# Kernel tuning notes

Measured on AMD Instinct MI355X. Metric: run time of the kernel, lower is better.

Reference implementation:

```python
import jax, jax.numpy as jnp
import numpy as np

EPS = 1e-5  # torch BatchNorm1d default eps
HEADS = 4


def knn_idx(pcd, K):
    # pcd: (B, N, C). Torch: topk of negative squared distance -> nearest K (includes self).
    aa = jnp.sum(pcd * pcd, axis=-1)                       # (B, N)
    inner = jnp.einsum('bnc,bmc->bnm', pcd, pcd)           # (B, N, N)
    pd = 2.0 * inner - aa[:, :, None] - aa[:, None, :]     # = -||a-b||^2
    return jax.lax.top_k(pd, K)[1]                         # (B, N, K) int32


def batchnorm1d(x, gamma, beta):
    # training-mode BN over (B, C, N): stats over batch and point dims, biased var
    m = jnp.mean(x, axis=(0, 2), keepdims=True)
    v = jnp.var(x, axis=(0, 2), keepdims=True)
    return (x - m) * jax.lax.rsqrt(v + EPS) * gamma[None, :, None] + beta[None, :, None]


def setup_inputs() -> dict:
    key = jax.random.key(0)
    ks = jax.random.split(key, 8)
    B, C, N = 4, 64, 8192
    FF = 4 * C  # 256
    x = jax.random.normal(ks[0], (B, C, N), dtype=jnp.float32)
    s = 1.0 / np.sqrt(C).astype(np.float32)
    Wq = jax.random.normal(ks[1], (C, C), dtype=jnp.float32) * s
    Wk = jax.random.normal(ks[2], (C, C), dtype=jnp.float32) * s
    Wv = jax.random.normal(ks[3], (C, C), dtype=jnp.float32) * s
    W1 = jax.random.normal(ks[4], (FF, C), dtype=jnp.float32) * s
    W2 = jax.random.normal(ks[5], (C, FF), dtype=jnp.float32) * (1.0 / np.sqrt(FF).astype(np.float32))
    g1 = jnp.ones((C,), jnp.float32); b1 = jnp.zeros((C,), jnp.float32)
    g2 = jnp.ones((C,), jnp.float32); b2 = jnp.zeros((C,), jnp.float32)
    return {'x': x, 'Wq': Wq, 'Wk': Wk, 'Wv': Wv, 'W1': W1, 'W2': W2,
            'g1': g1, 'b1': b1, 'g2': g2, 'b2': b2, 'K': 40}


def reference(x, Wq, Wk, Wv, W1, W2, g1, b1, g2, b2, K):
    B, C, N = x.shape
    H = HEADS
    D = C // H
    pcd = jnp.transpose(x, (0, 2, 1))                      # (B, N, C)
    idx = knn_idx(pcd, K)                                  # (B, N, K)
    nbr = jax.vmap(lambda p, i: p[i])(pcd, idx)            # (B, N, K, C) gather
    diff = nbr - pcd[:, :, None, :]                        # group_type='diff'
    # 1x1 conv projections
    q = jnp.einsum('oc,bnc->bno', Wq, pcd)                 # (B, N, C)
    k = jnp.einsum('oc,bnkc->bnko', Wk, diff)              # (B, N, K, C)
    v = jnp.einsum('oc,bnkc->bnko', Wv, diff)
    # split heads: channel = (H D), H-major
    qh = q.reshape(B, N, H, D)
    kh = k.reshape(B, N, K, H, D)
    vh = v.reshape(B, N, K, H, D)
    scale = np.float32(np.sqrt(D))
    energy = jnp.einsum('bnhd,bnkhd->bnhk', qh, kh) / scale
    attn = jax.nn.softmax(energy, axis=-1)
    out = jnp.einsum('bnhk,bnkhd->bnhd', attn, vh)         # (B, N, H, D)
    tmp = jnp.transpose(out.reshape(B, N, C), (0, 2, 1))   # (B, C, N)
    x1 = batchnorm1d(x + tmp, g1, b1)
    h = jax.nn.leaky_relu(jnp.einsum('oc,bcn->bon', W1, x1), 0.2)
    ff = jnp.einsum('co,bon->bcn', W2, h)
    return batchnorm1d(x1 + ff, g2, b2)
```

## Files before the change

kernel.cpp:

```cpp
#include <hip/hip_runtime.h>

#define Bc 4
#define Cc 64
#define Nc 8192
#define Kc 40
#define CN (Cc * Nc)

__global__ __launch_bounds__(256) void aa_kernel(const float* __restrict__ x,
                                                 float* __restrict__ aa) {
  const int e = blockIdx.x * 256 + threadIdx.x;
  const int b = e >> 13, n = e & 8191;
  const float* xb = x + (size_t)b * CN + n;
  float s = 0.f;
#pragma unroll
  for (int c = 0; c < 64; ++c) {
    const float v = xb[c * Nc];
    s = fmaf(v, v, s);
  }
  aa[e] = s;
}

__global__ __launch_bounds__(256) void proj_kernel(
    const float* __restrict__ x, const float* __restrict__ Wq,
    const float* __restrict__ Wk, const float* __restrict__ Wv,
    float* __restrict__ qp, float* __restrict__ kp, float* __restrict__ vp) {
  __shared__ float xs[64 * 64];
  __shared__ float wt[64 * 64];
  const int t = threadIdx.x;
  const int w = t >> 6, lane = t & 63;
  const int b = blockIdx.x >> 7;
  const int n0 = (blockIdx.x & 127) << 6;
  const float* xb = x + (size_t)b * CN;
  for (int c = w; c < 64; c += 4) xs[c * 64 + lane] = xb[c * Nc + n0 + lane];

  const float* Ws[3] = {Wq, Wk, Wv};
  float* Ds[3] = {qp, kp, vp};
  for (int mtx = 0; mtx < 3; ++mtx) {
    __syncthreads();
    const float* W = Ws[mtx];
    for (int q = t; q < 4096; q += 256) {
      const int o = q & 63, c = q >> 6;
      wt[c * 64 + o] = W[o * 64 + c];
    }
    __syncthreads();
    float acc[16];
#pragma unroll
    for (int k = 0; k < 16; ++k) acc[k] = 0.f;
#pragma unroll 8
    for (int c = 0; c < 64; ++c) {
      const float xv = xs[c * 64 + lane];
      const float4 w0 = *(const float4*)&wt[c * 64 + w * 16 + 0];
      const float4 w1 = *(const float4*)&wt[c * 64 + w * 16 + 4];
      const float4 w2 = *(const float4*)&wt[c * 64 + w * 16 + 8];
      const float4 w3 = *(const float4*)&wt[c * 64 + w * 16 + 12];
      acc[0] = fmaf(xv, w0.x, acc[0]);   acc[1] = fmaf(xv, w0.y, acc[1]);
      acc[2] = fmaf(xv, w0.z, acc[2]);   acc[3] = fmaf(xv, w0.w, acc[3]);
      acc[4] = fmaf(xv, w1.x, acc[4]);   acc[5] = fmaf(xv, w1.y, acc[5]);
      acc[6] = fmaf(xv, w1.z, acc[6]);   acc[7] = fmaf(xv, w1.w, acc[7]);
      acc[8] = fmaf(xv, w2.x, acc[8]);   acc[9] = fmaf(xv, w2.y, acc[9]);
      acc[10] = fmaf(xv, w2.z, acc[10]); acc[11] = fmaf(xv, w2.w, acc[11]);
      acc[12] = fmaf(xv, w3.x, acc[12]); acc[13] = fmaf(xv, w3.y, acc[13]);
      acc[14] = fmaf(xv, w3.z, acc[14]); acc[15] = fmaf(xv, w3.w, acc[15]);
    }
    float* dst = Ds[mtx] + ((size_t)(b * Nc + n0 + lane)) * 64 + w * 16;
    *(float4*)(dst + 0) = make_float4(acc[0], acc[1], acc[2], acc[3]);
    *(float4*)(dst + 4) = make_float4(acc[4], acc[5], acc[6], acc[7]);
    *(float4*)(dst + 8) = make_float4(acc[8], acc[9], acc[10], acc[11]);
    *(float4*)(dst + 12) = make_float4(acc[12], acc[13], acc[14], acc[15]);
  }
}

__global__ __launch_bounds__(256, 1) void knn_kernel(const float* __restrict__ x,
                                                     const float* __restrict__ aa,
                                                     int* __restrict__ knn) {
  __shared__ float rowT[64][128];
  __shared__ float colT[64][128];
  __shared__ float qv[128][64];
  __shared__ unsigned short qidx[128][64];
  __shared__ float thrS[128][2];
  __shared__ int qcnt[128];

  const int t = threadIdx.x;
  const int ty = t >> 4;
  const int tx = t & 15;
  const int b = blockIdx.x >> 6;
  const int i0 = (blockIdx.x & 63) << 7;
  const float* xb = x + (size_t)b * CN;
  const float* aab = aa + b * Nc;

  if (t < 128) { qcnt[t] = 0; thrS[t][0] = -INFINITY; thrS[t][1] = -INFINITY; }

  const int cSub = t >> 4;
  const int chunk = t & 15;
  for (int cc = 0; cc < 4; ++cc) {
    const int c = cc * 16 + cSub;
    const float* src = xb + (size_t)c * Nc + i0 + chunk * 8;
    const float4 v0 = ((const float4*)src)[0];
    const float4 v1 = ((const float4*)src)[1];
    *(float4*)&rowT[c][chunk * 8] = v0;
    *(float4*)&rowT[c][chunk * 8 + 4] = v1;
  }

  float rA[8];
  {
    const float4 r0 = *(const float4*)&aab[i0 + ty * 8];
    const float4 r1 = *(const float4*)&aab[i0 + ty * 8 + 4];
    rA[0] = r0.x; rA[1] = r0.y; rA[2] = r0.z; rA[3] = r0.w;
    rA[4] = r1.x; rA[5] = r1.y; rA[6] = r1.z; rA[7] = r1.w;
  }

  float lv[40]; int li[40];
#pragma unroll
  for (int q = 0; q < 40; ++q) { lv[q] = -INFINITY; li[q] = 0; }
  float lmin = -INFINITY; int lminpos = 0;

  const int dr = t >> 1, slot = t & 1;

  auto insert = [&](float v, int idx) {
#pragma unroll
    for (int q = 0; q < 40; ++q)
      if (q == lminpos) { lv[q] = v; li[q] = idx; }
    float nm = lv[0]; int np = 0;
#pragma unroll
    for (int q = 1; q < 40; ++q) {
      if (lv[q] < nm) { nm = lv[q]; np = q; }
    }
    lmin = nm; lminpos = np;
  };

  for (int jt = 0; jt < 64; ++jt) {
    const int j0 = jt << 7;
    for (int cc = 0; cc < 4; ++cc) {
      const int c = cc * 16 + cSub;
      const float* src = xb + (size_t)c * Nc + j0 + chunk * 8;
      const float4 v0 = ((const float4*)src)[0];
      const float4 v1 = ((const float4*)src)[1];
      *(float4*)&colT[c][chunk * 8] = v0;
      *(float4*)&colT[c][chunk * 8 + 4] = v1;
    }
    __syncthreads();

    float acc[8][8];
#pragma unroll
    for (int i = 0; i < 8; ++i)
#pragma unroll
      for (int jj = 0; jj < 8; ++jj) acc[i][jj] = 0.f;

#pragma unroll 2
    for (int c = 0; c < 64; ++c) {
      const float4 a0 = *(const float4*)&rowT[c][ty * 8];
      const float4 a1 = *(const float4*)&rowT[c][ty * 8 + 4];
      const float4 b0 = *(const float4*)&colT[c][tx * 4];
      const float4 b1 = *(const float4*)&colT[c][64 + tx * 4];
      const float av[8] = {a0.x, a0.y, a0.z, a0.w, a1.x, a1.y, a1.z, a1.w};
      const float bv[8] = {b0.x, b0.y, b0.z, b0.w, b1.x, b1.y, b1.z, b1.w};
#pragma unroll
      for (int i = 0; i < 8; ++i)
#pragma unroll
        for (int jj = 0; jj < 8; ++jj)
          acc[i][jj] = fmaf(av[i], bv[jj], acc[i][jj]);
    }

    float cA[8];
    {
      const float4 c0 = *(const float4*)&aab[j0 + tx * 4];
      const float4 c1 = *(const float4*)&aab[j0 + 64 + tx * 4];
      cA[0] = c0.x; cA[1] = c0.y; cA[2] = c0.z; cA[3] = c0.w;
      cA[4] = c1.x; cA[5] = c1.y; cA[6] = c1.z; cA[7] = c1.w;
    }

    for (int half = 0; half < 2; ++half) {
      float th8[8];
      {
        const float4* tp = (const float4*)&thrS[ty * 8][0];
        const float4 u0 = tp[0], u1 = tp[1], u2 = tp[2], u3 = tp[3];
        th8[0] = fminf(u0.x, u0.y); th8[1] = fminf(u0.z, u0.w);
        th8[2] = fminf(u1.x, u1.y); th8[3] = fminf(u1.z, u1.w);
        th8[4] = fminf(u2.x, u2.y); th8[5] = fminf(u2.z, u2.w);
        th8[6] = fminf(u3.x, u3.y); th8[7] = fminf(u3.z, u3.w);
      }
#pragma unroll
      for (int i = 0; i < 8; ++i) {
        const int r = ty * 8 + i;
#pragma unroll
        for (int jq = 0; jq < 4; ++jq) {
          const int jj = half * 4 + jq;
          const float v = 2.0f * acc[i][jj] - rA[i] - cA[jj];
          if (v > th8[i]) {
            const int pos = atomicAdd(&qcnt[r], 1);
            qv[r][pos] = v;
            qidx[r][pos] = (unsigned short)(j0 + half * 64 + tx * 4 + jq);
          }
        }
      }
      __syncthreads();
      {
        int cnt = qcnt[dr]; if (cnt > 64) cnt = 64;
        for (int e = slot; e < cnt; e += 2) {
          const float v = qv[dr][e];
          if (v > lmin) insert(v, (int)qidx[dr][e]);
        }
        if (slot == 0) qcnt[dr] = 0;
        thrS[dr][slot] = lmin;
      }
      __syncthreads();
    }
  }

  if (slot == 1) {
#pragma unroll
    for (int q = 0; q < 40; ++q) {
      qv[dr][q] = lv[q];
      qidx[dr][q] = (unsigned short)li[q];
    }
  }
  __syncthreads();
  if (slot == 0) {
#pragma unroll
    for (int q = 0; q < 40; ++q) {
      const float v = qv[dr][q];
      if (v > lmin) insert(v, (int)qidx[dr][q]);
    }
    int* dst = knn + (size_t)(b * Nc + i0 + dr) * Kc;
#pragma unroll
    for (int q = 0; q < 40; ++q) dst[q] = li[q];
  }
}

__global__ __launch_bounds__(256) void attn_kernel(
    const float* __restrict__ x, const float* __restrict__ qp,
    const float* __restrict__ kp, const float* __restrict__ vp,
    const int* __restrict__ knn, float* __restrict__ y) {
  const int lane = threadIdx.x & 63;
  const int wid = threadIdx.x >> 6;
  const int pt = (blockIdx.x << 2) + wid;
  const int b = pt >> 13;
  const int nn = pt & 8191;
  const float q = qp[(size_t)pt * 64 + lane];
  const float vself = vp[(size_t)pt * 64 + lane];
  const float* kpb = kp + (size_t)b * (Nc * 64);
  const float* vpb = vp + (size_t)b * (Nc * 64);
  const int* idn = knn + (size_t)pt * Kc;
  float e[40], vv[40];
#pragma unroll
  for (int j = 0; j < 40; ++j) {
    const int ij = idn[j];
    const float kj = kpb[ij * 64 + lane];
    vv[j] = vpb[ij * 64 + lane];
    float p = q * kj;
    p += __shfl_xor(p, 1);
    p += __shfl_xor(p, 2);
    p += __shfl_xor(p, 4);
    p += __shfl_xor(p, 8);
    e[j] = p * 0.25f;
  }
  float m = e[0];
#pragma unroll
  for (int j = 1; j < 40; ++j) m = fmaxf(m, e[j]);
  float s = 0.f;
#pragma unroll
  for (int j = 0; j < 40; ++j) { e[j] = __expf(e[j] - m); s += e[j]; }
  const float inv = 1.f / s;
  float acc = 0.f;
#pragma unroll
  for (int j = 0; j < 40; ++j) acc = fmaf(e[j] * inv, vv[j], acc);
  const size_t xi = (size_t)b * CN + (size_t)lane * Nc + nn;
  y[xi] = x[xi] + (acc - vself);
}

__global__ __launch_bounds__(256) void stats_kernel(const float* __restrict__ src,
                                                    float* __restrict__ out) {
  const int c = blockIdx.x;
  float s = 0.f, s2 = 0.f;
  for (int b = 0; b < Bc; ++b) {
    const float* p = src + (size_t)b * CN + (size_t)c * Nc;
    for (int i = threadIdx.x; i < Nc; i += 256) {
      const float v = p[i];
      s += v;
      s2 = fmaf(v, v, s2);
    }
  }
  __shared__ float rs[256], rs2[256];
  rs[threadIdx.x] = s; rs2[threadIdx.x] = s2;
  __syncthreads();
  for (int st = 128; st > 0; st >>= 1) {
    if (threadIdx.x < st) {
      rs[threadIdx.x] += rs[threadIdx.x + st];
      rs2[threadIdx.x] += rs2[threadIdx.x + st];
    }
    __syncthreads();
  }
  if (threadIdx.x == 0) {
    const float mean = rs[0] * (1.f / 32768.f);
    const float var = rs2[0] * (1.f / 32768.f) - mean * mean;
    out[c] = mean;
    out[64 + c] = 1.f / sqrtf(var + 1e-5f);
  }
}

__global__ __launch_bounds__(256) void w2t_kernel(const float* __restrict__ W2,
                                                  float* __restrict__ W2t) {
  const int e = blockIdx.x * 256 + threadIdx.x;
  const int o = e >> 6, c = e & 63;
  W2t[e] = W2[c * 256 + o];
}

__global__ __launch_bounds__(256) void ffn_kernel(
    const float* __restrict__ y, const float* __restrict__ W1,
    const float* __restrict__ W2t, const float* __restrict__ st1,
    const float* __restrict__ g1, const float* __restrict__ b1,
    float* __restrict__ z) {
  const int pt = blockIdx.x * 256 + threadIdx.x;
  const int b = pt >> 13, nn = pt & 8191;
  const float* yb = y + (size_t)b * CN + nn;
  float x1[64], z0[64];
#pragma unroll
  for (int c = 0; c < 64; ++c) {
    const float sc = st1[64 + c] * g1[c];
    x1[c] = (yb[(size_t)c * Nc] - st1[c]) * sc + b1[c];
    z0[c] = x1[c];
  }
  for (int o = 0; o < 256; ++o) {
    const float* w1r = W1 + o * 64;
    float hv = 0.f;
#pragma unroll
    for (int c = 0; c < 64; ++c) hv = fmaf(w1r[c], x1[c], hv);
    hv = hv >= 0.f ? hv : 0.2f * hv;
    const float* w2r = W2t + o * 64;
#pragma unroll
    for (int c = 0; c < 64; ++c) z0[c] = fmaf(w2r[c], hv, z0[c]);
  }
  float* zb = z + (size_t)b * CN + nn;
#pragma unroll
  for (int c = 0; c < 64; ++c) zb[(size_t)c * Nc] = z0[c];
}

__global__ __launch_bounds__(256) void bn_apply_kernel(
    const float* __restrict__ z, const float* __restrict__ st2,
    const float* __restrict__ g2, const float* __restrict__ b2,
    float* __restrict__ out) {
  const int e = blockIdx.x * 256 + threadIdx.x;
  const int c = (e >> 13) & 63;
  const float sc = st2[64 + c] * g2[c];
  out[e] = (z[e] - st2[c]) * sc + b2[c];
}

extern "C" void kernel_launch(void* const* d_in, const int* in_sizes, int n_in,
                              void* d_out, int out_size, void* d_ws, size_t ws_size,
                              hipStream_t stream) {
  (void)in_sizes; (void)n_in; (void)out_size; (void)ws_size;
  const float* x  = (const float*)d_in[0];
  const float* Wq = (const float*)d_in[1];
  const float* Wk = (const float*)d_in[2];
  const float* Wv = (const float*)d_in[3];
  const float* W1 = (const float*)d_in[4];
  const float* W2 = (const float*)d_in[5];
  const float* g1 = (const float*)d_in[6];
  const float* b1 = (const float*)d_in[7];
  const float* g2 = (const float*)d_in[8];
  const float* b2 = (const float*)d_in[9];
  float* out = (float*)d_out;

  float* ws = (float*)d_ws;
  float* aa  = ws;
  float* qp  = aa + 32768;
  float* kp  = qp + 2097152;
  float* vp  = kp + 2097152;
  float* y   = vp + 2097152;
  float* z   = y + 2097152;
  float* st1 = z + 2097152;
  float* st2 = st1 + 128;
  float* W2t = st2 + 128;
  int* knn   = (int*)(W2t + 16384);

  hipLaunchKernelGGL(aa_kernel, dim3(128), dim3(256), 0, stream, x, aa);
  hipLaunchKernelGGL(proj_kernel, dim3(512), dim3(256), 0, stream, x, Wq, Wk, Wv, qp, kp, vp);
  hipLaunchKernelGGL(knn_kernel, dim3(256), dim3(256), 0, stream, x, aa, knn);
  hipLaunchKernelGGL(attn_kernel, dim3(8192), dim3(256), 0, stream, x, qp, kp, vp, knn, y);
  hipLaunchKernelGGL(stats_kernel, dim3(64), dim3(256), 0, stream, y, st1);
  hipLaunchKernelGGL(w2t_kernel, dim3(64), dim3(256), 0, stream, W2, W2t);
  hipLaunchKernelGGL(ffn_kernel, dim3(128), dim3(256), 0, stream, y, W1, W2t, st1, g1, b1, z);
  hipLaunchKernelGGL(stats_kernel, dim3(64), dim3(256), 0, stream, z, st2);
  hipLaunchKernelGGL(bn_apply_kernel, dim3(8192), dim3(256), 0, stream, z, st2, g2, b2, out);
}
```

Measured before the change: 1.840 ms.

## Split KNN search over column halves with merge kernel, prefetch and wave-level queues

Splits the KNN search so each block scans half of the candidate columns, which doubles the grid to 512 blocks and allows two blocks per CU. Partial top-40 lists go to scratch memory reused from the y and z buffers, and a new merge kernel combines them. Inside the loop, the next column tile is prefetched into registers. Candidate insertion now builds a per-thread bitmask, drains it in eight rounds separated by wave barriers instead of block barriers, and uses smaller per-row queues. The cost is extra global traffic and a launch for the merge, plus heavier register pressure under launch_bounds(256,2). The 16-entry queue also relies on each round adding at most 16 candidates per row.

New measurement: 3.208 ms. 1.74x slower.

```diff
diff --git a/kernel.cpp b/kernel.cpp
--- a/kernel.cpp
+++ b/kernel.cpp
@@ -70,35 +70,39 @@
   }
 }
 
-__global__ __launch_bounds__(256, 1) void knn_kernel(const float* __restrict__ x,
+__global__ __launch_bounds__(256, 2) void knn_kernel(const float* __restrict__ x,
                                                      const float* __restrict__ aa,
-                                                     int* __restrict__ knn) {
+                                                     float* __restrict__ part_v,
+                                                     unsigned short* __restrict__ part_i) {
   __shared__ float rowT[64][128];
   __shared__ float colT[64][128];
-  __shared__ float qv[128][64];
-  __shared__ unsigned short qidx[128][64];
+  __shared__ float qv[128][16];
+  __shared__ unsigned short qidx[128][16];
   __shared__ float thrS[128][2];
   __shared__ int qcnt[128];
 
   const int t = threadIdx.x;
   const int ty = t >> 4;
   const int tx = t & 15;
-  const int b = blockIdx.x >> 6;
-  const int i0 = (blockIdx.x & 63) << 7;
+  const int blk = blockIdx.x;
+  const int h = blk & 1;
+  const int i0 = ((blk >> 1) & 63) << 7;
+  const int b = blk >> 7;
+  const int j0base = h * 4096;
   const float* xb = x + (size_t)b * CN;
   const float* aab = aa + b * Nc;
 
   if (t < 128) { qcnt[t] = 0; thrS[t][0] = -INFINITY; thrS[t][1] = -INFINITY; }
 
-  const int cSub = t >> 4;
-  const int chunk = t & 15;
-  for (int cc = 0; cc < 4; ++cc) {
-    const int c = cc * 16 + cSub;
-    const float* src = xb + (size_t)c * Nc + i0 + chunk * 8;
-    const float4 v0 = ((const float4*)src)[0];
-    const float4 v1 = ((const float4*)src)[1];
-    *(float4*)&rowT[c][chunk * 8] = v0;
-    *(float4*)&rowT[c][chunk * 8 + 4] = v1;
+#pragma unroll
+  for (int k = 0; k < 8; ++k) {
+    const int c = k * 8 + (t >> 5), j = (t & 31) * 4;
+    *(float4*)&rowT[c][j] = *(const float4*)&xb[(size_t)c * Nc + i0 + j];
+  }
+#pragma unroll
+  for (int k = 0; k < 8; ++k) {
+    const int c = k * 8 + (t >> 5), j = (t & 31) * 4;
+    *(float4*)&colT[c][j] = *(const float4*)&xb[(size_t)c * Nc + j0base + j];
   }
 
   float rA[8];
@@ -113,7 +117,6 @@
 #pragma unroll
   for (int q = 0; q < 40; ++q) { lv[q] = -INFINITY; li[q] = 0; }
   float lmin = -INFINITY; int lminpos = 0;
-
   const int dr = t >> 1, slot = t & 1;
 
   auto insert = [&](float v, int idx) {
@@ -128,17 +131,20 @@
     lmin = nm; lminpos = np;
   };
 
-  for (int jt = 0; jt < 64; ++jt) {
-    const int j0 = jt << 7;
-    for (int cc = 0; cc < 4; ++cc) {
-      const int c = cc * 16 + cSub;
-      const float* src = xb + (size_t)c * Nc + j0 + chunk * 8;
-      const float4 v0 = ((const float4*)src)[0];
-      const float4 v1 = ((const float4*)src)[1];
-      *(float4*)&colT[c][chunk * 8] = v0;
-      *(float4*)&colT[c][chunk * 8 + 4] = v1;
-    }
-    __syncthreads();
+  __syncthreads();
+
+  for (int jt = 0; jt < 32; ++jt) {
+    const int j0 = j0base + (jt << 7);
+
+    float4 pf[8];
+    if (jt < 31) {
+      const int nj0 = j0 + 128;
+#pragma unroll
+      for (int k = 0; k < 8; ++k) {
+        const int c = k * 8 + (t >> 5), j = (t & 31) * 4;
+        pf[k] = *(const float4*)&xb[(size_t)c * Nc + nj0 + j];
+      }
+    }
 
     float acc[8][8];
 #pragma unroll
@@ -169,33 +175,42 @@
       cA[4] = c1.x; cA[5] = c1.y; cA[6] = c1.z; cA[7] = c1.w;
     }
 
-    for (int half = 0; half < 2; ++half) {
-      float th8[8];
-      {
-        const float4* tp = (const float4*)&thrS[ty * 8][0];
-        const float4 u0 = tp[0], u1 = tp[1], u2 = tp[2], u3 = tp[3];
-        th8[0] = fminf(u0.x, u0.y); th8[1] = fminf(u0.z, u0.w);
-        th8[2] = fminf(u1.x, u1.y); th8[3] = fminf(u1.z, u1.w);
-        th8[4] = fminf(u2.x, u2.y); th8[5] = fminf(u2.z, u2.w);
-        th8[6] = fminf(u3.x, u3.y); th8[7] = fminf(u3.z, u3.w);
-      }
-#pragma unroll
-      for (int i = 0; i < 8; ++i) {
-        const int r = ty * 8 + i;
-#pragma unroll
-        for (int jq = 0; jq < 4; ++jq) {
-          const int jj = half * 4 + jq;
-          const float v = 2.0f * acc[i][jj] - rA[i] - cA[jj];
-          if (v > th8[i]) {
-            const int pos = atomicAdd(&qcnt[r], 1);
-            qv[r][pos] = v;
-            qidx[r][pos] = (unsigned short)(j0 + half * 64 + tx * 4 + jq);
+    float th8[8];
+#pragma unroll
+    for (int i = 0; i < 8; ++i)
+      th8[i] = fminf(thrS[ty * 8 + i][0], thrS[ty * 8 + i][1]);
+
+    unsigned long long mask = 0ull;
+#pragma unroll
+    for (int i = 0; i < 8; ++i)
+#pragma unroll
+      for (int jj = 0; jj < 8; ++jj) {
+        const float v = 2.0f * acc[i][jj] - rA[i] - cA[jj];
+        if (v > th8[i]) mask |= (1ull << (i * 8 + jj));
+      }
+
+#pragma unroll 1
+    for (int p = 0; p < 8; ++p) {
+      const int quad = p >> 2;
+      if ((tx >> 2) == (p & 3) && mask) {
+#pragma unroll
+        for (int i = 0; i < 8; ++i) {
+#pragma unroll
+          for (int jq = 0; jq < 4; ++jq) {
+            const int jj = quad * 4 + jq;
+            if ((mask >> (i * 8 + jj)) & 1ull) {
+              const float v = 2.0f * acc[i][jj] - rA[i] - cA[jj];
+              const int r = ty * 8 + i;
+              const int pos = atomicAdd(&qcnt[r], 1);
+              qv[r][pos] = v;
+              qidx[r][pos] = (unsigned short)(j0 + quad * 64 + tx * 4 + jq);
+            }
           }
         }
       }
-      __syncthreads();
+      __builtin_amdgcn_wave_barrier();
       {
-        int cnt = qcnt[dr]; if (cnt > 64) cnt = 64;
+        int cnt = qcnt[dr]; if (cnt > 16) cnt = 16;
         for (int e = slot; e < cnt; e += 2) {
           const float v = qv[dr][e];
           if (v > lmin) insert(v, (int)qidx[dr][e]);
@@ -203,28 +218,70 @@
         if (slot == 0) qcnt[dr] = 0;
         thrS[dr][slot] = lmin;
       }
-      __syncthreads();
-    }
-  }
-
+      __builtin_amdgcn_wave_barrier();
+    }
+
+    __syncthreads();
+    if (jt < 31) {
+#pragma unroll
+      for (int k = 0; k < 8; ++k) {
+        const int c = k * 8 + (t >> 5), j = (t & 31) * 4;
+        *(float4*)&colT[c][j] = pf[k];
+      }
+    }
+    __syncthreads();
+  }
+
+  float* shv = &rowT[0][0];
+  int* shi = (int*)&colT[0][0];
   if (slot == 1) {
 #pragma unroll
-    for (int q = 0; q < 40; ++q) {
-      qv[dr][q] = lv[q];
-      qidx[dr][q] = (unsigned short)li[q];
-    }
+    for (int q = 0; q < 40; ++q) { shv[dr * 40 + q] = lv[q]; shi[dr * 40 + q] = li[q]; }
   }
   __syncthreads();
   if (slot == 0) {
 #pragma unroll
     for (int q = 0; q < 40; ++q) {
-      const float v = qv[dr][q];
-      if (v > lmin) insert(v, (int)qidx[dr][q]);
-    }
-    int* dst = knn + (size_t)(b * Nc + i0 + dr) * Kc;
-#pragma unroll
-    for (int q = 0; q < 40; ++q) dst[q] = li[q];
-  }
+      const float v = shv[dr * 40 + q];
+      if (v > lmin) insert(v, shi[dr * 40 + q]);
+    }
+    const size_t base = ((size_t)(b * Nc + i0 + dr) * 2 + h) * 40;
+#pragma unroll
+    for (int q = 0; q < 40; ++q) {
+      part_v[base + q] = lv[q];
+      part_i[base + q] = (unsigned short)li[q];
+    }
+  }
+}
+
+__global__ __launch_bounds__(256) void knn_merge_kernel(const float* __restrict__ part_v,
+                                                        const unsigned short* __restrict__ part_i,
+                                                        int* __restrict__ knn) {
+  const int row = blockIdx.x * 256 + threadIdx.x;
+  float lv[40]; int li[40];
+#pragma unroll
+  for (int q = 0; q < 40; ++q) { lv[q] = -INFINITY; li[q] = 0; }
+  float lmin = -INFINITY; int lminpos = 0;
+  const float* pv = part_v + (size_t)row * 80;
+  const unsigned short* pi = part_i + (size_t)row * 80;
+  for (int e = 0; e < 80; ++e) {
+    const float v = pv[e];
+    if (v > lmin) {
+      const int idx = (int)pi[e];
+#pragma unroll
+      for (int q = 0; q < 40; ++q)
+        if (q == lminpos) { lv[q] = v; li[q] = idx; }
+      float nm = lv[0]; int np = 0;
+#pragma unroll
+      for (int q = 1; q < 40; ++q) {
+        if (lv[q] < nm) { nm = lv[q]; np = q; }
+      }
+      lmin = nm; lminpos = np;
+    }
+  }
+  int* dst = knn + (size_t)row * Kc;
+#pragma unroll
+  for (int q = 0; q < 40; ++q) dst[q] = li[q];
 }
 
 __global__ __launch_bounds__(256) void attn_kernel(
@@ -372,10 +429,13 @@
   float* st2 = st1 + 128;
   float* W2t = st2 + 128;
   int* knn   = (int*)(W2t + 16384);
+  float* partv = y;
+  unsigned short* parti = (unsigned short*)(z + 524288);
 
   hipLaunchKernelGGL(aa_kernel, dim3(128), dim3(256), 0, stream, x, aa);
   hipLaunchKernelGGL(proj_kernel, dim3(512), dim3(256), 0, stream, x, Wq, Wk, Wv, qp, kp, vp);
-  hipLaunchKernelGGL(knn_kernel, dim3(256), dim3(256), 0, stream, x, aa, knn);
+  hipLaunchKernelGGL(knn_kernel, dim3(512), dim3(256), 0, stream, x, aa, partv, parti);
+  hipLaunchKernelGGL(knn_merge_kernel, dim3(128), dim3(256), 0, stream, partv, parti, knn);
   hipLaunchKernelGGL(attn_kernel, dim3(8192), dim3(256), 0, stream, x, qp, kp, vp, knn, y);
   hipLaunchKernelGGL(stats_kernel, dim3(64), dim3(256), 0, stream, y, st1);
   hipLaunchKernelGGL(w2t_kernel, dim3(64), dim3(256), 0, stream, W2, W2t);
```
